# Performance work log

Measured on AMD Instinct MI355X. Metric: run time of the kernel, lower is better.

The kernel has to match this reference:

```python
import jax, jax.numpy as jnp
import numpy as np

D_L, D_A, D_V = 711, 300, 74
H = 64  # dh_l = dh_a = dh_v = mem_dim
ATT_IN = 2 * 3 * H      # 384 (windowsize=2 * total_h_dim)
GAMMA_IN = ATT_IN + H   # 448
FINAL = 3 * H + H       # 256


def _lstm(x, h, c, wih, whh):
    # torch LSTMCell (bias=False): gate order i, f, g, o
    gates = x @ wih + h @ whh
    i, f, g, o = jnp.split(gates, 4, axis=1)
    i = jax.nn.sigmoid(i)
    f = jax.nn.sigmoid(f)
    o = jax.nn.sigmoid(o)
    g = jnp.tanh(g)
    c_new = f * c + i * g
    return o * jnp.tanh(c_new), c_new


def setup_inputs() -> dict:
    key = jax.random.key(0)
    ks = jax.random.split(key, 32)
    def w(k, shape, s=0.08):
        return jax.random.normal(k, shape, dtype=jnp.float32) * s
    B, T = 256, 200
    inp = {"x": jax.random.normal(ks[0], (B, T, D_L + D_A + D_V), dtype=jnp.float32)}
    # LSTM weights stored [in, 4H] / [H, 4H] so we use x @ W (torch uses x @ W_ih.T)
    inp["w_ih_l"] = w(ks[1], (D_L, 4 * H)); inp["w_hh_l"] = w(ks[2], (H, 4 * H))
    inp["w_ih_a"] = w(ks[3], (D_A, 4 * H)); inp["w_hh_a"] = w(ks[4], (H, 4 * H))
    inp["w_ih_v"] = w(ks[5], (D_V, 4 * H)); inp["w_hh_v"] = w(ks[6], (H, 4 * H))
    inp["att1_w1"] = w(ks[7], (ATT_IN, H));  inp["att1_b1"] = jnp.zeros((H,), jnp.float32)
    inp["att1_w2"] = w(ks[8], (H, ATT_IN));  inp["att1_b2"] = jnp.zeros((ATT_IN,), jnp.float32)
    inp["att2_w1"] = w(ks[9], (ATT_IN, H));  inp["att2_b1"] = jnp.zeros((H,), jnp.float32)
    inp["att2_w2"] = w(ks[10], (H, H));      inp["att2_b2"] = jnp.zeros((H,), jnp.float32)
    inp["g1_w1"] = w(ks[11], (GAMMA_IN, H)); inp["g1_b1"] = jnp.zeros((H,), jnp.float32)
    inp["g1_w2"] = w(ks[12], (H, H));        inp["g1_b2"] = jnp.zeros((H,), jnp.float32)
    inp["g2_w1"] = w(ks[13], (GAMMA_IN, H)); inp["g2_b1"] = jnp.zeros((H,), jnp.float32)
    inp["g2_w2"] = w(ks[14], (H, H));        inp["g2_b2"] = jnp.zeros((H,), jnp.float32)
    inp["out_w1"] = w(ks[15], (FINAL, H))
    inp["out_w2"] = w(ks[16], (H, 1))
    return inp


def reference(x, w_ih_l, w_hh_l, w_ih_a, w_hh_a, w_ih_v, w_hh_v,
              att1_w1, att1_b1, att1_w2, att1_b2,
              att2_w1, att2_b1, att2_w2, att2_b2,
              g1_w1, g1_b1, g1_w2, g1_b2,
              g2_w1, g2_b1, g2_w2, g2_b2,
              out_w1, out_w2):
    # dropout layers act as identity (eval mode)
    xs = jnp.transpose(x, (1, 0, 2))  # [T, B, D]
    x_l = xs[:, :, :D_L]
    x_a = xs[:, :, D_L:D_L + D_A]
    x_v = xs[:, :, D_L + D_A:]
    B = x.shape[0]
    z = jnp.zeros((B, H), dtype=x.dtype)
    carry0 = (z, z, z, z, z, z, z)  # h_l, h_a, h_v, c_l, c_a, c_v, mem

    def step(carry, xt):
        h_l, h_a, h_v, c_l, c_a, c_v, mem = carry
        xl, xa, xv = xt
        nh_l, nc_l = _lstm(xl, h_l, c_l, w_ih_l, w_hh_l)
        nh_a, nc_a = _lstm(xa, h_a, c_a, w_ih_a, w_hh_a)
        nh_v, nc_v = _lstm(xv, h_v, c_v, w_ih_v, w_hh_v)
        prev_cs = jnp.concatenate([c_l, c_a, c_v], axis=1)
        new_cs = jnp.concatenate([nc_l, nc_a, nc_v], axis=1)
        c_star = jnp.concatenate([prev_cs, new_cs], axis=1)  # [B, 384]
        attention = jax.nn.softmax(
            jax.nn.relu(c_star @ att1_w1 + att1_b1) @ att1_w2 + att1_b2, axis=1)
        attended = attention * c_star
        c_hat = jnp.tanh(
            jax.nn.relu(attended @ att2_w1 + att2_b1) @ att2_w2 + att2_b2)
        both = jnp.concatenate([attended, mem], axis=1)  # [B, 448]
        gamma1 = jax.nn.sigmoid(jax.nn.relu(both @ g1_w1 + g1_b1) @ g1_w2 + g1_b2)
        gamma2 = jax.nn.sigmoid(jax.nn.relu(both @ g2_w1 + g2_b1) @ g2_w2 + g2_b2)
        mem_new = gamma1 * mem + gamma2 * c_hat
        return (nh_l, nh_a, nh_v, nc_l, nc_a, nc_v, mem_new), None

    (h_l, h_a, h_v, _, _, _, mem), _ = jax.lax.scan(step, carry0, (x_l, x_a, x_v))
    last_hs = jnp.concatenate([h_l, h_a, h_v, mem], axis=1)  # [B, 256]
    return jax.nn.relu(last_hs @ out_w1) @ out_w2  # [B, 1]
```

## Files before the change

### kernel.cpp

```cpp
#include <hip/hip_runtime.h>
#include <hip/hip_bf16.h>
#include <cstdint>
#include <cstddef>

#define HH 64
#define BB 256
#define TT 200
#define DL 711
#define DA 300
#define DV 74
#define DD 1085
#define GXW 768
#define NROW (TT * BB)
#define HPOFF ((size_t)NROW * GXW)


__global__ __launch_bounds__(256) void proj_kernel(
    const float* __restrict__ x,
    const float* __restrict__ wl,
    const float* __restrict__ wa,
    const float* __restrict__ wv,
    float* __restrict__ gx)
{
    const int mod = blockIdx.y;
    const int K   = (mod == 0) ? DL : (mod == 1 ? DA : DV);
    const int off = (mod == 0) ? 0  : (mod == 1 ? DL : (DL + DA));
    const float* __restrict__ W = (mod == 0) ? wl : (mod == 1 ? wa : wv);

    const int tid = threadIdx.x;
    const int r0  = blockIdx.x * 64;

    __shared__ float As[32][65];
    __shared__ float Bs[32][256];

    const int tm = (tid >> 5) << 3;
    const int tn = (tid & 31) << 3;

    const int am = tid >> 2;
    const int ad = (tid & 3) << 3;
    const int r  = r0 + am;
    const int b  = r & 255;
    const int t  = r >> 8;
    const float* __restrict__ xrow = x + ((size_t)b * TT + t) * DD + off;

    const int bk = tid >> 3;
    const int bf = tid & 7;

    float acc[8][8];
    #pragma unroll
    for (int i = 0; i < 8; ++i)
        #pragma unroll
        for (int j = 0; j < 8; ++j) acc[i][j] = 0.f;

    for (int k0 = 0; k0 < K; k0 += 32) {
        #pragma unroll
        for (int u = 0; u < 8; ++u) {
            int d = k0 + ad + u;
            As[ad + u][am] = (d < K) ? xrow[d] : 0.f;
        }
        {
            const bool kin = (k0 + bk) < K;
            const float4* __restrict__ wrow4 =
                (const float4*)(W + (size_t)(k0 + bk) * 256);
            #pragma unroll
            for (int u = 0; u < 8; ++u) {
                int c4 = bf + u * 8;
                float4 v = kin ? wrow4[c4] : make_float4(0.f, 0.f, 0.f, 0.f);
                *(float4*)&Bs[bk][c4 << 2] = v;
            }
        }
        __syncthreads();

        #pragma unroll
        for (int kk = 0; kk < 32; ++kk) {
            float a[8], bb[8];
            #pragma unroll
            for (int i = 0; i < 8; ++i) a[i] = As[kk][tm + i];
            float4 b0 = *(const float4*)&Bs[kk][tn];
            float4 b1 = *(const float4*)&Bs[kk][tn + 4];
            bb[0] = b0.x; bb[1] = b0.y; bb[2] = b0.z; bb[3] = b0.w;
            bb[4] = b1.x; bb[5] = b1.y; bb[6] = b1.z; bb[7] = b1.w;
            #pragma unroll
            for (int i = 0; i < 8; ++i)
                #pragma unroll
                for (int j = 0; j < 8; ++j)
                    acc[i][j] += a[i] * bb[j];
        }
        __syncthreads();
    }

    #pragma unroll
    for (int i = 0; i < 8; ++i) {
        size_t row = (size_t)(r0 + tm + i);
        float* o = gx + row * GXW + mod * 256 + tn;
        *(float4*)&o[0] = make_float4(acc[i][0], acc[i][1], acc[i][2], acc[i][3]);
        *(float4*)&o[4] = make_float4(acc[i][4], acc[i][5], acc[i][6], acc[i][7]);
    }
}

__global__ __launch_bounds__(256) void lstm_kernel(
    float* gx,
    const float* __restrict__ whhl,
    const float* __restrict__ whha,
    const float* __restrict__ whhv,
    const float* __restrict__ ow1,
    float* __restrict__ hp)
{
    const int m   = blockIdx.x;
    const int b0  = blockIdx.y * 8;
    const int tid = threadIdx.x;
    const float* __restrict__ W = (m == 0) ? whhl : ((m == 1) ? whha : whhv);

    __shared__ float h[8][64];
    __shared__ float c[8][64];
    __shared__ float gb[8][256];

    for (int i = tid; i < 512; i += 256) { ((float*)h)[i] = 0.f; ((float*)c)[i] = 0.f; }
    __syncthreads();

    for (int t = 0; t < TT; ++t) {
        {
            const int k = tid;
            const float* gxt = gx + ((size_t)(t * BB + b0)) * GXW + m * 256 + k;
            float s[8];
            #pragma unroll
            for (int r = 0; r < 8; ++r) s[r] = gxt[(size_t)r * GXW];
            #pragma unroll 16
            for (int i = 0; i < 64; ++i) {
                float w = W[i * 256 + k];
                #pragma unroll
                for (int r = 0; r < 8; ++r) s[r] += h[r][i] * w;
            }
            #pragma unroll
            for (int r = 0; r < 8; ++r) gb[r][k] = s[r];
        }
        __syncthreads();
        {
            const int j = tid & 63, rr = tid >> 6;
            #pragma unroll
            for (int u = 0; u < 2; ++u) {
                const int r = rr + u * 4;
                float ig = gb[r][j];
                float fg = gb[r][j + 64];
                float gg = gb[r][j + 128];
                float og = gb[r][j + 192];
                float iv = 1.f / (1.f + expf(-ig));
                float fv = 1.f / (1.f + expf(-fg));
                float ov = 1.f / (1.f + expf(-og));
                float gv = tanhf(gg);
                float co = c[r][j];
                float cn = fv * co + iv * gv;
                float* grow = gx + ((size_t)(t * BB + b0 + r)) * GXW + m * 256;
                grow[j]      = co;
                grow[64 + j] = cn;
                c[r][j] = cn;
                h[r][j] = ov * tanhf(cn);
            }
        }
        __syncthreads();
    }

    {
        const int j = tid & 63, rr = tid >> 6;
        #pragma unroll
        for (int u = 0; u < 2; ++u) {
            const int r = rr + u * 4;
            float s = 0.f;
            for (int i = 0; i < 64; ++i)
                s += h[r][i] * ow1[(m * 64 + i) * 64 + j];
            hp[((size_t)m * BB + b0 + r) * 64 + j] = s;
        }
    }
}

__global__ __launch_bounds__(256) void att_kernel(
    float* gx,
    const float* __restrict__ a1w1, const float* __restrict__ a1b1,
    const float* __restrict__ a1w2, const float* __restrict__ a1b2,
    const float* __restrict__ a2w1, const float* __restrict__ a2b1,
    const float* __restrict__ a2w2, const float* __restrict__ a2b2,
    const float* __restrict__ g1w1, const float* __restrict__ g1b1,
    const float* __restrict__ g2w1, const float* __restrict__ g2b1)
{
    const int tid = threadIdx.x;
    const size_t R0 = (size_t)blockIdx.x * 32;

    __shared__ float cs[32][384];
    __shared__ float hb[32][64];

    for (int u = 0; u < 48; ++u) {
        int flat = tid + u * 256;
        int rr = flat / 384;
        int i  = flat - rr * 384;
        int col;
        if (i < 192) col = (i >> 6) * 256 + (i & 63);
        else { int jj = i - 192; col = (jj >> 6) * 256 + 64 + (jj & 63); }
        cs[rr][i] = gx[(R0 + rr) * GXW + col];
    }
    __syncthreads();

    const int j   = tid & 63;
    const int rrg = tid >> 6;

    {
        float acc[8];
        #pragma unroll
        for (int u = 0; u < 8; ++u) acc[u] = a1b1[j];
        for (int i = 0; i < 384; ++i) {
            float w = a1w1[i * 64 + j];
            #pragma unroll
            for (int u = 0; u < 8; ++u) acc[u] += cs[rrg * 8 + u][i] * w;
        }
        #pragma unroll
        for (int u = 0; u < 8; ++u) hb[rrg * 8 + u][j] = fmaxf(acc[u], 0.f);
    }
    __syncthreads();

    {
        const int lane = tid & 63;
        float sc[6][8];
        #pragma unroll
        for (int q = 0; q < 6; ++q) {
            float bv = a1b2[lane + q * 64];
            #pragma unroll
            for (int u = 0; u < 8; ++u) sc[q][u] = bv;
        }
        for (int i = 0; i < 64; ++i) {
            float av[8];
            #pragma unroll
            for (int u = 0; u < 8; ++u) av[u] = hb[rrg * 8 + u][i];
            #pragma unroll
            for (int q = 0; q < 6; ++q) {
                float w = a1w2[i * 384 + lane + q * 64];
                #pragma unroll
                for (int u = 0; u < 8; ++u) sc[q][u] += av[u] * w;
            }
        }
        #pragma unroll
        for (int u = 0; u < 8; ++u) {
            const int r = rrg * 8 + u;
            float mx = sc[0][u];
            #pragma unroll
            for (int q = 1; q < 6; ++q) mx = fmaxf(mx, sc[q][u]);
            #pragma unroll
            for (int o = 32; o > 0; o >>= 1) mx = fmaxf(mx, __shfl_xor(mx, o));
            float sm = 0.f;
            float e[6];
            #pragma unroll
            for (int q = 0; q < 6; ++q) { e[q] = expf(sc[q][u] - mx); sm += e[q]; }
            #pragma unroll
            for (int o = 32; o > 0; o >>= 1) sm += __shfl_xor(sm, o);
            float inv = 1.f / sm;
            #pragma unroll
            for (int q = 0; q < 6; ++q) {
                int L = lane + q * 64;
                cs[r][L] = e[q] * inv * cs[r][L];
            }
        }
    }
    __syncthreads();

    {
        float sa[8], s1[8], s2[8];
        #pragma unroll
        for (int u = 0; u < 8; ++u) { sa[u] = a2b1[j]; s1[u] = g1b1[j]; s2[u] = g2b1[j]; }
        for (int i = 0; i < 384; ++i) {
            float wa = a2w1[i * 64 + j];
            float w1 = g1w1[i * 64 + j];
            float w2 = g2w1[i * 64 + j];
            #pragma unroll
            for (int u = 0; u < 8; ++u) {
                float v = cs[rrg * 8 + u][i];
                sa[u] += v * wa; s1[u] += v * w1; s2[u] += v * w2;
            }
        }
        #pragma unroll
        for (int u = 0; u < 8; ++u) {
            const size_t r = R0 + rrg * 8 + u;
            float* grow = gx + r * GXW;
            grow[384 + j] = s1[u];
            grow[448 + j] = s2[u];
            hb[rrg * 8 + u][j] = fmaxf(sa[u], 0.f);
        }
    }
    __syncthreads();

    {
        float acc[8];
        #pragma unroll
        for (int u = 0; u < 8; ++u) acc[u] = a2b2[j];
        for (int i = 0; i < 64; ++i) {
            float w = a2w2[i * 64 + j];
            #pragma unroll
            for (int u = 0; u < 8; ++u) acc[u] += hb[rrg * 8 + u][i] * w;
        }
        #pragma unroll
        for (int u = 0; u < 8; ++u)
            gx[(R0 + rrg * 8 + u) * GXW + 192 + j] = tanhf(acc[u]);
    }
}

__global__ __launch_bounds__(64) void mem_kernel(
    const float* __restrict__ gx,
    const float* __restrict__ g1w1, const float* __restrict__ g1w2, const float* __restrict__ g1b2,
    const float* __restrict__ g2w1, const float* __restrict__ g2w2, const float* __restrict__ g2b2,
    const float* __restrict__ ow1,  const float* __restrict__ ow2,
    const float* __restrict__ hp,
    float* __restrict__ out)
{
    const int j = threadIdx.x;
    const int b = blockIdx.x;

    __shared__ float Wm1[64][64];
    __shared__ float Wm2[64][64];
    __shared__ float Wf1[64][64];
    __shared__ float Wf2[64][64];

    for (int i = 0; i < 64; ++i) {
        Wm1[i][j] = g1w1[(384 + i) * 64 + j];
        Wm2[i][j] = g2w1[(384 + i) * 64 + j];
        Wf1[i][j] = g1w2[i * 64 + j];
        Wf2[i][j] = g2w2[i * 64 + j];
    }
    const float bf1 = g1b2[j], bf2 = g2b2[j];
    __syncthreads();

    float mem = 0.f;
    const float* base0 = gx + (size_t)b * GXW;
    float cj = base0[192 + j];
    float p1 = base0[384 + j];
    float p2 = base0[448 + j];

    for (int t = 0; t < TT; ++t) {
        float ncj = 0.f, np1 = 0.f, np2 = 0.f;
        if (t + 1 < TT) {
            const float* nb = gx + ((size_t)(t + 1) * BB + b) * GXW;
            ncj = nb[192 + j]; np1 = nb[384 + j]; np2 = nb[448 + j];
        }
        float s1 = p1, s2 = p2;
        #pragma unroll 8
        for (int i = 0; i < 64; ++i) {
            float mv = __shfl(mem, i);
            s1 += mv * Wm1[i][j];
            s2 += mv * Wm2[i][j];
        }
        float h1 = fmaxf(s1, 0.f);
        float h2 = fmaxf(s2, 0.f);
        float t1 = bf1, t2 = bf2;
        #pragma unroll 8
        for (int i = 0; i < 64; ++i) {
            t1 += __shfl(h1, i) * Wf1[i][j];
            t2 += __shfl(h2, i) * Wf2[i][j];
        }
        float g1 = 1.f / (1.f + expf(-t1));
        float g2 = 1.f / (1.f + expf(-t2));
        mem = g1 * mem + g2 * cj;
        cj = ncj; p1 = np1; p2 = np2;
    }

    float s = hp[((size_t)0 * BB + b) * 64 + j]
            + hp[((size_t)1 * BB + b) * 64 + j]
            + hp[((size_t)2 * BB + b) * 64 + j];
    #pragma unroll 8
    for (int i = 0; i < 64; ++i)
        s += __shfl(mem, i) * ow1[(192 + i) * 64 + j];
    float y = fmaxf(s, 0.f) * ow2[j];
    #pragma unroll
    for (int o = 32; o > 0; o >>= 1) y += __shfl_xor(y, o);
    if (j == 0) out[b] = y;
}

extern "C" void kernel_launch(void* const* d_in, const int* in_sizes, int n_in,
                              void* d_out, int out_size, void* d_ws, size_t ws_size,
                              hipStream_t stream)
{
    const float* x    = (const float*)d_in[0];
    const float* wihl = (const float*)d_in[1];
    const float* whhl = (const float*)d_in[2];
    const float* wiha = (const float*)d_in[3];
    const float* whha = (const float*)d_in[4];
    const float* wihv = (const float*)d_in[5];
    const float* whhv = (const float*)d_in[6];
    const float* a1w1 = (const float*)d_in[7];
    const float* a1b1 = (const float*)d_in[8];
    const float* a1w2 = (const float*)d_in[9];
    const float* a1b2 = (const float*)d_in[10];
    const float* a2w1 = (const float*)d_in[11];
    const float* a2b1 = (const float*)d_in[12];
    const float* a2w2 = (const float*)d_in[13];
    const float* a2b2 = (const float*)d_in[14];
    const float* g1w1 = (const float*)d_in[15];
    const float* g1b1 = (const float*)d_in[16];
    const float* g1w2 = (const float*)d_in[17];
    const float* g1b2 = (const float*)d_in[18];
    const float* g2w1 = (const float*)d_in[19];
    const float* g2b1 = (const float*)d_in[20];
    const float* g2w2 = (const float*)d_in[21];
    const float* g2b2 = (const float*)d_in[22];
    const float* ow1  = (const float*)d_in[23];
    const float* ow2  = (const float*)d_in[24];

    float* gx  = (float*)d_ws;
    float* hp  = (float*)d_ws + HPOFF;
    float* out = (float*)d_out;

    proj_kernel<<<dim3(800, 3, 1), dim3(256, 1, 1), 0, stream>>>(
        x, wihl, wiha, wihv, gx);

    lstm_kernel<<<dim3(3, 32, 1), dim3(256, 1, 1), 0, stream>>>(
        gx, whhl, whha, whhv, ow1, hp);

    att_kernel<<<dim3(1600, 1, 1), dim3(256, 1, 1), 0, stream>>>(
        gx,
        a1w1, a1b1, a1w2, a1b2,
        a2w1, a2b1, a2w2, a2b2,
        g1w1, g1b1, g2w1, g2b1);

    mem_kernel<<<dim3(256, 1, 1), dim3(64, 1, 1), 0, stream>>>(
        gx, g1w1, g1w2, g1b2, g2w1, g2w2, g2b2, ow1, ow2, hp, out);
}
```

Before: 2.822 ms.

## Restructure LSTM recurrence into single-wavefront blocks with shuffle-broadcast hidden state

The LSTM recurrence kernel now runs 384 blocks of 64 threads (one wavefront), each handling 2 batch rows of one modality, instead of 96 blocks of 256 threads handling 8 rows. The recurrent weights are staged once in LDS as float4 per gate column. The hidden state lives in registers and is broadcast with wave shuffles, which removes the per-step __syncthreads and shared gate buffer. The next timestep's input projections are prefetched during the current step. This targets the serial latency of the 200-step recurrence and the low occupancy of the old grid, at the cost of reusing each loaded weight across fewer batch rows.

New measurement: 3.630 ms. 28.6% more time.

```diff
diff --git a/kernel.cpp b/kernel.cpp
--- a/kernel.cpp
+++ b/kernel.cpp
@@ -98,7 +98,7 @@
     }
 }
 
-__global__ __launch_bounds__(256) void lstm_kernel(
+__global__ __launch_bounds__(64) void lstm_kernel(
     float* gx,
     const float* __restrict__ whhl,
     const float* __restrict__ whha,
@@ -106,70 +106,83 @@
     const float* __restrict__ ow1,
     float* __restrict__ hp)
 {
-    const int m   = blockIdx.x;
-    const int b0  = blockIdx.y * 8;
-    const int tid = threadIdx.x;
+    const int blk = blockIdx.x;
+    const int m   = blk >> 7;
+    const int b0  = (blk & 127) * 2;
+    const int j   = threadIdx.x;
     const float* __restrict__ W = (m == 0) ? whhl : ((m == 1) ? whha : whhv);
 
-    __shared__ float h[8][64];
-    __shared__ float c[8][64];
-    __shared__ float gb[8][256];
-
-    for (int i = tid; i < 512; i += 256) { ((float*)h)[i] = 0.f; ((float*)c)[i] = 0.f; }
-    __syncthreads();
+    __shared__ float4 Wi[64][64];
+    #pragma unroll 4
+    for (int i = 0; i < 64; ++i) {
+        const float* wr = W + i * 256 + j;
+        Wi[i][j] = make_float4(wr[0], wr[64], wr[128], wr[192]);
+    }
+
+    float h0 = 0.f, h1 = 0.f, c0 = 0.f, c1 = 0.f;
+
+    float g0[4], g1[4];
+    {
+        const float* p = gx + ((size_t)b0) * GXW + m * 256 + j;
+        #pragma unroll
+        for (int g = 0; g < 4; ++g) { g0[g] = p[g * 64]; g1[g] = p[GXW + g * 64]; }
+    }
 
     for (int t = 0; t < TT; ++t) {
-        {
-            const int k = tid;
-            const float* gxt = gx + ((size_t)(t * BB + b0)) * GXW + m * 256 + k;
-            float s[8];
-            #pragma unroll
-            for (int r = 0; r < 8; ++r) s[r] = gxt[(size_t)r * GXW];
-            #pragma unroll 16
-            for (int i = 0; i < 64; ++i) {
-                float w = W[i * 256 + k];
-                #pragma unroll
-                for (int r = 0; r < 8; ++r) s[r] += h[r][i] * w;
-            }
-            #pragma unroll
-            for (int r = 0; r < 8; ++r) gb[r][k] = s[r];
-        }
-        __syncthreads();
-        {
-            const int j = tid & 63, rr = tid >> 6;
-            #pragma unroll
-            for (int u = 0; u < 2; ++u) {
-                const int r = rr + u * 4;
-                float ig = gb[r][j];
-                float fg = gb[r][j + 64];
-                float gg = gb[r][j + 128];
-                float og = gb[r][j + 192];
-                float iv = 1.f / (1.f + expf(-ig));
-                float fv = 1.f / (1.f + expf(-fg));
-                float ov = 1.f / (1.f + expf(-og));
-                float gv = tanhf(gg);
-                float co = c[r][j];
-                float cn = fv * co + iv * gv;
-                float* grow = gx + ((size_t)(t * BB + b0 + r)) * GXW + m * 256;
-                grow[j]      = co;
-                grow[64 + j] = cn;
-                c[r][j] = cn;
-                h[r][j] = ov * tanhf(cn);
-            }
-        }
-        __syncthreads();
-    }
-
-    {
-        const int j = tid & 63, rr = tid >> 6;
-        #pragma unroll
-        for (int u = 0; u < 2; ++u) {
-            const int r = rr + u * 4;
-            float s = 0.f;
-            for (int i = 0; i < 64; ++i)
-                s += h[r][i] * ow1[(m * 64 + i) * 64 + j];
-            hp[((size_t)m * BB + b0 + r) * 64 + j] = s;
-        }
+        float a0[4], a1[4];
+        #pragma unroll
+        for (int g = 0; g < 4; ++g) { a0[g] = g0[g]; a1[g] = g1[g]; }
+
+        #pragma unroll
+        for (int i = 0; i < 64; ++i) {
+            float4 wv = Wi[i][j];
+            float hv0 = __shfl(h0, i);
+            float hv1 = __shfl(h1, i);
+            a0[0] += hv0 * wv.x; a0[1] += hv0 * wv.y;
+            a0[2] += hv0 * wv.z; a0[3] += hv0 * wv.w;
+            a1[0] += hv1 * wv.x; a1[1] += hv1 * wv.y;
+            a1[2] += hv1 * wv.z; a1[3] += hv1 * wv.w;
+        }
+
+        if (t + 1 < TT) {
+            const float* p = gx + ((size_t)(t + 1) * BB + b0) * GXW + m * 256 + j;
+            #pragma unroll
+            for (int g = 0; g < 4; ++g) { g0[g] = p[g * 64]; g1[g] = p[GXW + g * 64]; }
+        }
+
+        float iv0 = 1.f / (1.f + expf(-a0[0]));
+        float fv0 = 1.f / (1.f + expf(-a0[1]));
+        float gv0 = tanhf(a0[2]);
+        float ov0 = 1.f / (1.f + expf(-a0[3]));
+        float iv1 = 1.f / (1.f + expf(-a1[0]));
+        float fv1 = 1.f / (1.f + expf(-a1[1]));
+        float gv1 = tanhf(a1[2]);
+        float ov1 = 1.f / (1.f + expf(-a1[3]));
+
+        float cn0 = fv0 * c0 + iv0 * gv0;
+        float cn1 = fv1 * c1 + iv1 * gv1;
+
+        float* grow = gx + ((size_t)t * BB + b0) * GXW + m * 256;
+        grow[j]            = c0;
+        grow[64 + j]       = cn0;
+        grow[GXW + j]      = c1;
+        grow[GXW + 64 + j] = cn1;
+
+        c0 = cn0; c1 = cn1;
+        h0 = ov0 * tanhf(cn0);
+        h1 = ov1 * tanhf(cn1);
+    }
+
+    {
+        float s0 = 0.f, s1 = 0.f;
+        #pragma unroll 8
+        for (int i = 0; i < 64; ++i) {
+            float w = ow1[(m * 64 + i) * 64 + j];
+            s0 += __shfl(h0, i) * w;
+            s1 += __shfl(h1, i) * w;
+        }
+        hp[((size_t)m * BB + b0) * 64 + j]     = s0;
+        hp[((size_t)m * BB + b0 + 1) * 64 + j] = s1;
     }
 }
 
@@ -407,7 +420,7 @@
     proj_kernel<<<dim3(800, 3, 1), dim3(256, 1, 1), 0, stream>>>(
         x, wihl, wiha, wihv, gx);
 
-    lstm_kernel<<<dim3(3, 32, 1), dim3(256, 1, 1), 0, stream>>>(
+    lstm_kernel<<<dim3(384, 1, 1), dim3(64, 1, 1), 0, stream>>>(
         gx, whhl, whha, whhv, ow1, hp);
 
     att_kernel<<<dim3(1600, 1, 1), dim3(256, 1, 1), 0, stream>>>(
```
